# Kernel optimization log

Hardware: AMD Instinct MI355X
Metric: run time of the kernel (lower is better)

Reference implementation:

```python
import jax, jax.numpy as jnp
import numpy as np

D_MODEL = 512
D_STATE = 16
EXPAND = 2
DT_RANK = 8
D_INNER = EXPAND * D_MODEL  # 1024
LN_EPS = 1e-5


def setup_inputs() -> dict:
    key = jax.random.key(0)
    ks = jax.random.split(key, 10)
    B, H, W = 8, 48, 48
    inp = {
        "x": jax.random.normal(ks[0], (B, H, W, D_MODEL), jnp.float32),
        # Linear weights stored [in, out] (torch weight transposed)
        "W_in": jax.random.normal(ks[1], (D_MODEL, 2 * D_INNER), jnp.float32) * 0.02,
        # depthwise conv kernel, HWIO with feature_group_count = D_INNER
        "conv_k": jax.random.normal(ks[2], (3, 3, 1, D_INNER), jnp.float32) * 0.1,
        "W_xproj": jax.random.normal(ks[3], (D_INNER, DT_RANK + 2 * D_STATE), jnp.float32) * 0.02,
        "W_dt": jax.random.uniform(ks[4], (DT_RANK, D_INNER), jnp.float32, -0.1, 0.1),
        "b_dt": jnp.full((D_INNER,), 0.1, jnp.float32),
        "A_log": jax.random.normal(ks[5], (D_STATE,), jnp.float32) * 0.02,
        "Dskip": jnp.ones((D_INNER,), jnp.float32),
        "W_dtN": jax.random.normal(ks[6], (D_INNER, D_STATE), jnp.float32) * 0.02,
        "b_dtN": jnp.zeros((D_STATE,), jnp.float32),
        "ln_g": jnp.ones((D_INNER,), jnp.float32),
        "ln_b": jnp.zeros((D_INNER,), jnp.float32),
        "W_out": jax.random.normal(ks[7], (D_INNER, D_MODEL), jnp.float32) * 0.02,
        "b_out": jnp.zeros((D_MODEL,), jnp.float32),
    }
    return inp


def _ss2d(x, W_in, conv_k, W_xproj, W_dt, b_dt, A_log, Dskip, W_dtN, b_dtN,
          ln_g, ln_b, W_out, b_out):
    B, H, W_, _ = x.shape
    L = H * W_
    # in_proj and split into x / gate z
    xz = x @ W_in                                   # [B,H,W,2*D_INNER]
    xh, z = jnp.split(xz, 2, axis=-1)
    # depthwise 3x3 conv (NHWC)
    xc = jax.lax.conv_general_dilated(
        xh, conv_k, window_strides=(1, 1), padding='SAME',
        dimension_numbers=('NHWC', 'HWIO', 'NHWC'),
        feature_group_count=D_INNER)                 # [B,H,W,D_INNER]
    # x_proj -> (dt_rank, B, C)
    xp = xc @ W_xproj
    dt_r = xp[..., :DT_RANK]
    Bp = xp[..., DT_RANK:DT_RANK + D_STATE]
    Cp = xp[..., DT_RANK + D_STATE:]
    dt = dt_r @ W_dt + b_dt                          # [B,H,W,D_INNER]
    # flatten spatial dims into sequence
    x_seq = xc.reshape(B, L, D_INNER)
    dt_seq = jax.nn.softplus(dt.reshape(B, L, D_INNER))
    B_seq = Bp.reshape(B, L, D_STATE)
    C_seq = Cp.reshape(B, L, D_STATE)
    A = -jnp.exp(A_log)                              # [N]; A_log expanded over D is constant per-row
    dtN = dt_seq @ W_dtN + b_dtN                     # dt_to_N_proj(softplus(dt)) -> [B,L,N]

    def step(h, t):
        x_t, dt_t, dtN_t, B_t, C_t = t               # [B,D],[B,D],[B,N],[B,N],[B,N]
        dA = jnp.exp(dt_t[:, :, None] * A)           # [B,D,N]
        dB = dtN_t * B_t                             # [B,N]
        h = dA * h + dB[:, None, :] * x_t[:, :, None]  # [B,D,N]
        y = jnp.einsum('bdn,bn->bd', h, C_t) + Dskip * x_t
        return h, y

    h0 = jnp.zeros((B, D_INNER, D_STATE), x.dtype)
    xs = (x_seq.transpose(1, 0, 2), dt_seq.transpose(1, 0, 2),
          dtN.transpose(1, 0, 2), B_seq.transpose(1, 0, 2),
          C_seq.transpose(1, 0, 2))
    _, ys = jax.lax.scan(step, h0, xs)               # ys: [L,B,D]
    y = ys.transpose(1, 0, 2).reshape(B, H, W_, D_INNER)
    # LayerNorm over channel dim
    mu = y.mean(-1, keepdims=True)
    var = ((y - mu) ** 2).mean(-1, keepdims=True)
    y = (y - mu) / jnp.sqrt(var + LN_EPS) * ln_g + ln_b
    # gate and out projection (dropout = identity in eval)
    y = y * jax.nn.silu(z)
    return y @ W_out + b_out


def reference(x, W_in, conv_k, W_xproj, W_dt, b_dt, A_log, Dskip, W_dtN,
              b_dtN, ln_g, ln_b, W_out, b_out):
    return _ss2d(x, W_in, conv_k, W_xproj, W_dt, b_dt, A_log, Dskip, W_dtN,
                 b_dtN, ln_g, ln_b, W_out, b_out)
```

## Files before the change

### kernel.cpp

```cpp
#include <hip/hip_runtime.h>
#include <hip/hip_bf16.h>

#define NBATCH 8
#define HEIGHT 48
#define WIDTH  48
#define DMODEL 512
#define DSTATE 16
#define DTRANK 8
#define DINNER 1024
#define LSEQ   (HEIGHT*WIDTH)
#define NROWS  (NBATCH*LSEQ)
#define NXP    40
#define NCH    64
#define TCH    36

typedef unsigned short u16;
typedef unsigned int   u32;
typedef __attribute__((ext_vector_type(8))) short short8;
typedef __attribute__((ext_vector_type(4))) float f32x4;

__device__ __forceinline__ float bf2f(u16 u) {
    u32 x = ((u32)u) << 16;
    return __uint_as_float(x);
}
__device__ __forceinline__ u16 f2bf(float f) {
    u32 x = __float_as_uint(f);
    u32 r = (x + 0x7FFFu + ((x >> 16) & 1u)) >> 16;
    return (u16)r;
}

#if __has_builtin(__builtin_amdgcn_exp2f)
__device__ __forceinline__ float EXP2(float x) { return __builtin_amdgcn_exp2f(x); }
#else
__device__ __forceinline__ float EXP2(float x) { return __expf(x * 0.69314718f); }
#endif

#define GLD16(g, l) __builtin_amdgcn_global_load_lds( \
    (const __attribute__((address_space(1))) void*)(g), \
    (__attribute__((address_space(3))) void*)(l), 16, 0, 0)

__global__ __launch_bounds__(256) void k_prep(const float* __restrict__ x,
                                              const float* __restrict__ W_in,
                                              const float* __restrict__ W_out,
                                              const float* __restrict__ W_xproj,
                                              const float* __restrict__ W_dtN,
                                              u16* __restrict__ xbf,
                                              u16* __restrict__ WinT,
                                              u16* __restrict__ WoutT,
                                              u16* __restrict__ WxpB,
                                              u16* __restrict__ WdtNB) {
    if (blockIdx.x < 9216) {
        int i = blockIdx.x * 256 + threadIdx.x;
        float4 v = *reinterpret_cast<const float4*>(x + (size_t)i * 4);
        ushort4 o;
        o.x = f2bf(v.x); o.y = f2bf(v.y); o.z = f2bf(v.z); o.w = f2bf(v.w);
        *reinterpret_cast<ushort4*>(xbf + (size_t)i * 4) = o;
        return;
    }
    int idx = (blockIdx.x - 9216) * 256 + threadIdx.x;
    if (idx < 2048 * 512) {
        int n = idx >> 9, k = idx & 511;
        WinT[idx] = f2bf(W_in[(size_t)k * 2048 + n]);
    } else if (idx < 2048 * 512 + 512 * 1024) {
        int j = idx - 2048 * 512;
        int n = j >> 10, k = j & 1023;
        WoutT[j] = f2bf(W_out[(size_t)k * 512 + n]);
    } else if (idx < 2048 * 512 + 512 * 1024 + 48 * 1024) {
        int j = idx - (2048 * 512 + 512 * 1024);
        int n = j >> 10, k = j & 1023;
        WxpB[j] = (n < NXP) ? f2bf(W_xproj[(size_t)k * NXP + n]) : (u16)0;
    } else {
        int j = idx - (2048 * 512 + 512 * 1024 + 48 * 1024);
        int n = j >> 10, k = j & 1023;
        WdtNB[j] = f2bf(W_dtN[(size_t)k * DSTATE + n]);
    }
}

template<int K, int LDA, int LDB, int LDC, bool F32OUT>
__global__ __launch_bounds__(256) void k_gemm_mfma(const u16* __restrict__ A,
                                                   const u16* __restrict__ B,
                                                   const float* __restrict__ bias,
                                                   void* __restrict__ Cv) {
    __shared__ u16 As[128 * 32];
    __shared__ u16 Bs[128 * 32];
    const int tid = threadIdx.x;
    const int l   = tid & 63;
    const int w   = tid >> 6;
    const int wm  = w >> 1, wn = w & 1;
    const int id   = blockIdx.y * gridDim.x + blockIdx.x;
    const int nwg  = gridDim.x * gridDim.y;
    const int swz  = (id & 7) * (nwg >> 3) + (id >> 3);
    const int bx   = swz % gridDim.x;
    const int by   = swz / gridDim.x;
    const int m0  = by * 128, n0 = bx * 128;
    const int srow = w * 32 + (l >> 2);
    const int sc   = l & 3;
    const int kh = l >> 4;
    const int lr = l & 15;

    f32x4 acc[4][4];
#pragma unroll
    for (int i = 0; i < 4; ++i)
#pragma unroll
        for (int j = 0; j < 4; ++j)
            acc[i][j] = (f32x4){0.f, 0.f, 0.f, 0.f};

    for (int k0 = 0; k0 < K; k0 += 32) {
#pragma unroll
        for (int i = 0; i < 2; ++i) {
            int r  = srow + i * 16;
            int cg = sc ^ ((r >> 1) & 3);
            const u16* ga = A + (size_t)(m0 + r) * LDA + k0 + cg * 8;
            const u16* gb = B + (size_t)(n0 + r) * LDB + k0 + cg * 8;
            GLD16(ga, As + (w * 2 + i) * 512);
            GLD16(gb, Bs + (w * 2 + i) * 512);
        }
        __syncthreads();
        short8 af[4], bfr[4];
#pragma unroll
        for (int f = 0; f < 4; ++f) {
            int ar = wm * 64 + f * 16 + lr;
            af[f]  = *reinterpret_cast<const short8*>(As + ar * 32 + ((kh ^ ((ar >> 1) & 3)) * 8));
            int br = wn * 64 + f * 16 + lr;
            bfr[f] = *reinterpret_cast<const short8*>(Bs + br * 32 + ((kh ^ ((br >> 1) & 3)) * 8));
        }
#pragma unroll
        for (int fm = 0; fm < 4; ++fm)
#pragma unroll
            for (int fn = 0; fn < 4; ++fn)
                acc[fm][fn] = __builtin_amdgcn_mfma_f32_16x16x32_bf16(
                    af[fm], bfr[fn], acc[fm][fn], 0, 0, 0);
        __syncthreads();
    }

#pragma unroll
    for (int fm = 0; fm < 4; ++fm) {
#pragma unroll
        for (int r = 0; r < 4; ++r) {
            int row = m0 + wm * 64 + fm * 16 + (l >> 4) * 4 + r;
#pragma unroll
            for (int fn = 0; fn < 4; ++fn) {
                int col = n0 + wn * 64 + fn * 16 + lr;
                if (F32OUT) {
                    ((float*)Cv)[(size_t)row * LDC + col] = acc[fm][fn][r] + bias[col];
                } else {
                    ((u16*)Cv)[(size_t)row * LDC + col] = f2bf(acc[fm][fn][r]);
                }
            }
        }
    }
}

__global__ __launch_bounds__(256) void k_conv(const u16* __restrict__ xz,
                                              const float* __restrict__ ck,
                                              u16* __restrict__ xc) {
    const int blk = blockIdx.x;
    const int wg = blk % (WIDTH / 8);
    const int hb = blk / (WIDTH / 8);
    const int h = hb % HEIGHT;
    const int b = hb / HEIGHT;
    const int w0 = wg * 8;
    const int c0 = threadIdx.x * 4;

    float acc[8][4];
#pragma unroll
    for (int j = 0; j < 8; ++j)
#pragma unroll
        for (int q = 0; q < 4; ++q) acc[j][q] = 0.f;

#pragma unroll
    for (int kh = 0; kh < 3; ++kh) {
        int hh = h + kh - 1;
        if (hh < 0 || hh >= HEIGHT) continue;
        const u16* rp = xz + ((size_t)(b * HEIGHT + hh) * WIDTH) * 2048 + c0;
        float a[10][4];
#pragma unroll
        for (int i = 0; i < 10; ++i) {
            int ww = w0 - 1 + i;
            if (ww >= 0 && ww < WIDTH) {
                ushort4 v = *reinterpret_cast<const ushort4*>(rp + (size_t)ww * 2048);
                a[i][0] = bf2f(v.x); a[i][1] = bf2f(v.y);
                a[i][2] = bf2f(v.z); a[i][3] = bf2f(v.w);
            } else {
                a[i][0] = a[i][1] = a[i][2] = a[i][3] = 0.f;
            }
        }
#pragma unroll
        for (int kw = 0; kw < 3; ++kw) {
            float4 kv = *reinterpret_cast<const float4*>(ck + (kh * 3 + kw) * DINNER + c0);
#pragma unroll
            for (int j = 0; j < 8; ++j) {
                acc[j][0] = fmaf(a[j + kw][0], kv.x, acc[j][0]);
                acc[j][1] = fmaf(a[j + kw][1], kv.y, acc[j][1]);
                acc[j][2] = fmaf(a[j + kw][2], kv.z, acc[j][2]);
                acc[j][3] = fmaf(a[j + kw][3], kv.w, acc[j][3]);
            }
        }
    }
    const size_t orow = (size_t)((b * HEIGHT + h) * WIDTH + w0);
#pragma unroll
    for (int j = 0; j < 8; ++j) {
        ushort4 ov;
        ov.x = f2bf(acc[j][0]); ov.y = f2bf(acc[j][1]);
        ov.z = f2bf(acc[j][2]); ov.w = f2bf(acc[j][3]);
        *reinterpret_cast<ushort4*>(xc + (orow + j) * DINNER + c0) = ov;
    }
}

__global__ __launch_bounds__(256) void k_xproj(const u16* __restrict__ xc,
                                               const u16* __restrict__ WxpB,
                                               float* __restrict__ xp_out) {
    __shared__ u16 As[64 * 32];
    __shared__ u16 Bs[48 * 32];
    const int tid = threadIdx.x;
    const int l = tid & 63;
    const int w = tid >> 6;
    const int m0 = blockIdx.x * 64;
    const int kh = l >> 4, lr = l & 15;
    const int srow = w * 16 + (l >> 2);
    const int sc = l & 3;

    f32x4 acc[3];
    acc[0] = acc[1] = acc[2] = (f32x4){0.f, 0.f, 0.f, 0.f};

    for (int k0 = 0; k0 < 1024; k0 += 32) {
        {
            int cg = sc ^ ((srow >> 1) & 3);
            GLD16(xc + (size_t)(m0 + srow) * DINNER + k0 + cg * 8, As + w * 512);
            if (w < 3)
                GLD16(WxpB + (size_t)srow * 1024 + k0 + cg * 8, Bs + w * 512);
        }
        __syncthreads();
        int ar = w * 16 + lr;
        short8 af = *reinterpret_cast<const short8*>(As + ar * 32 + ((kh ^ ((ar >> 1) & 3)) * 8));
#pragma unroll
        for (int fn = 0; fn < 3; ++fn) {
            int br = fn * 16 + lr;
            short8 bf = *reinterpret_cast<const short8*>(Bs + br * 32 + ((kh ^ ((br >> 1) & 3)) * 8));
            acc[fn] = __builtin_amdgcn_mfma_f32_16x16x32_bf16(af, bf, acc[fn], 0, 0, 0);
        }
        __syncthreads();
    }
#pragma unroll
    for (int fn = 0; fn < 3; ++fn)
#pragma unroll
        for (int r = 0; r < 4; ++r) {
            int row = m0 + w * 16 + (l >> 4) * 4 + r;
            int col = fn * 16 + lr;
            if (col < NXP) xp_out[(size_t)row * NXP + col] = acc[fn][r];
        }
}

__global__ __launch_bounds__(256) void k_dt(const float* __restrict__ xp,
                                            const float* __restrict__ W_dt,
                                            const float* __restrict__ b_dt,
                                            u16* __restrict__ dt_out) {
    int gid = blockIdx.x * 256 + threadIdx.x;
    int row = gid >> 7;
    int dj  = (gid & 127) * 8;
    const float* xr = xp + (size_t)row * NXP;
    float4 xa = *reinterpret_cast<const float4*>(xr);
    float4 xb = *reinterpret_cast<const float4*>(xr + 4);
    float xv[8] = {xa.x, xa.y, xa.z, xa.w, xb.x, xb.y, xb.z, xb.w};
    float a[8];
    {
        float4 b0 = *reinterpret_cast<const float4*>(b_dt + dj);
        float4 b1 = *reinterpret_cast<const float4*>(b_dt + dj + 4);
        a[0]=b0.x; a[1]=b0.y; a[2]=b0.z; a[3]=b0.w;
        a[4]=b1.x; a[5]=b1.y; a[6]=b1.z; a[7]=b1.w;
    }
#pragma unroll
    for (int j = 0; j < 8; ++j) {
        float4 w0 = *reinterpret_cast<const float4*>(W_dt + j * DINNER + dj);
        float4 w1 = *reinterpret_cast<const float4*>(W_dt + j * DINNER + dj + 4);
        a[0] = fmaf(xv[j], w0.x, a[0]); a[1] = fmaf(xv[j], w0.y, a[1]);
        a[2] = fmaf(xv[j], w0.z, a[2]); a[3] = fmaf(xv[j], w0.w, a[3]);
        a[4] = fmaf(xv[j], w1.x, a[4]); a[5] = fmaf(xv[j], w1.y, a[5]);
        a[6] = fmaf(xv[j], w1.z, a[6]); a[7] = fmaf(xv[j], w1.w, a[7]);
    }
    short8 o;
#pragma unroll
    for (int j = 0; j < 8; ++j) {
        float dt = fmaxf(a[j], 0.f) + log1pf(__expf(-fabsf(a[j])));
        o[j] = (short)f2bf(dt);
    }
    *reinterpret_cast<short8*>(dt_out + (size_t)row * DINNER + dj) = o;
}

__global__ __launch_bounds__(256) void k_dtn(const u16* __restrict__ dtb,
                                             const u16* __restrict__ WdtNB,
                                             const float* __restrict__ b_dtN,
                                             const float* __restrict__ xp,
                                             float* __restrict__ dnBC) {
    __shared__ u16 As[64 * 32];
    __shared__ u16 Bs[16 * 32];
    const int tid = threadIdx.x;
    const int l = tid & 63;
    const int w = tid >> 6;
    const int m0 = blockIdx.x * 64;
    const int kh = l >> 4, lr = l & 15;
    const int srow = w * 16 + (l >> 2);
    const int sc = l & 3;

    f32x4 acc = (f32x4){0.f, 0.f, 0.f, 0.f};

    for (int k0 = 0; k0 < 1024; k0 += 32) {
        {
            int cg = sc ^ ((srow >> 1) & 3);
            GLD16(dtb + (size_t)(m0 + srow) * DINNER + k0 + cg * 8, As + w * 512);
            if (w == 0)
                GLD16(WdtNB + (size_t)srow * 1024 + k0 + cg * 8, Bs);
        }
        __syncthreads();
        int ar = w * 16 + lr;
        short8 af = *reinterpret_cast<const short8*>(As + ar * 32 + ((kh ^ ((ar >> 1) & 3)) * 8));
        short8 bf = *reinterpret_cast<const short8*>(Bs + lr * 32 + ((kh ^ ((lr >> 1) & 3)) * 8));
        acc = __builtin_amdgcn_mfma_f32_16x16x32_bf16(af, bf, acc, 0, 0, 0);
        __syncthreads();
    }
    float bn = b_dtN[lr];
#pragma unroll
    for (int r = 0; r < 4; ++r) {
        int row = m0 + w * 16 + (l >> 4) * 4 + r;
        float dn = acc[r] + bn;
        float Bv = xp[(size_t)row * NXP + DTRANK + lr];
        float Cv = xp[(size_t)row * NXP + DTRANK + DSTATE + lr];
        dnBC[(size_t)row * 32 + lr]      = dn * Bv;
        dnBC[(size_t)row * 32 + 16 + lr] = Cv;
    }
}

#define P1_N(IDX, COMP) \
    dA = EXP2(dt * An2[IDX]); h[IDX] = fmaf(dA, h[IDX], COMP * xt);

#define P1_BODY(T, DTC, XCC, DTN, XCN, PR) { \
    const float4* sv = pS + (size_t)(T) * 8; \
    float4 u0 = sv[0], u1 = sv[1], u2 = sv[2], u3 = sv[3]; \
    if (PR) { DTN = pdt[(size_t)((T) + 1) * DINNER]; \
              XCN = pxc[(size_t)((T) + 1) * DINNER]; } \
    float dt = bf2f(DTC), xt = bf2f(XCC); \
    sdt += dt; \
    float dA; \
    P1_N(0,  u0.x) P1_N(1,  u0.y) P1_N(2,  u0.z) P1_N(3,  u0.w) \
    P1_N(4,  u1.x) P1_N(5,  u1.y) P1_N(6,  u1.z) P1_N(7,  u1.w) \
    P1_N(8,  u2.x) P1_N(9,  u2.y) P1_N(10, u2.z) P1_N(11, u2.w) \
    P1_N(12, u3.x) P1_N(13, u3.y) P1_N(14, u3.z) P1_N(15, u3.w) }

__global__ __launch_bounds__(256) void k_scan_p1(const u16* __restrict__ xc,
                                                 const u16* __restrict__ dtb,
                                                 const float* __restrict__ dnBC,
                                                 const float* __restrict__ A_log,
                                                 float* __restrict__ sdt_out,
                                                 float* __restrict__ Qbuf) {
    const int tid = threadIdx.x;
    const int id  = blockIdx.x;
    const int swz = (id & 7) * ((NBATCH * NCH * 4) >> 3) + (id >> 3);
    const int quarter = swz & 3;
    const int bc = swz >> 2;
    const int c = bc & (NCH - 1);
    const int b = bc >> 6;
    const int d = quarter * 256 + tid;

    float An2[16];
#pragma unroll
    for (int n = 0; n < 16; ++n)
        An2[n] = -__expf(A_log[n]) * 1.44269504f;

    float h[16];
#pragma unroll
    for (int n = 0; n < 16; ++n) h[n] = 0.f;
    float sdt = 0.f;

    const size_t row0 = (size_t)b * LSEQ + (size_t)c * TCH;
    const u16* pdt = dtb + row0 * DINNER + d;
    const u16* pxc = xc  + row0 * DINNER + d;
    const float4* pS = reinterpret_cast<const float4*>(dnBC + row0 * 32);

    u16 dtA = pdt[0], xcA = pxc[0];
    u16 dtB, xcB;

    for (int t = 0; t < TCH - 2; t += 2) {
        P1_BODY(t,     dtA, xcA, dtB, xcB, true)
        P1_BODY(t + 1, dtB, xcB, dtA, xcA, true)
    }
    P1_BODY(TCH - 2, dtA, xcA, dtB, xcB, true)
    P1_BODY(TCH - 1, dtB, xcB, dtA, xcA, false)

    sdt_out[(size_t)bc * DINNER + d] = sdt;
    size_t base = ((size_t)bc << 14) + d;
#pragma unroll
    for (int n = 0; n < 16; ++n)
        Qbuf[base + (size_t)n * DINNER] = h[n];
}

__global__ __launch_bounds__(256) void k_scan_p2(const float* __restrict__ sdt,
                                                 const float* __restrict__ A_log,
                                                 float* __restrict__ Qbuf) {
    int tid = blockIdx.x * 256 + threadIdx.x;
    int b = tid >> 14, rem = tid & 16383;
    int n = rem >> 10, d = rem & 1023;
    float An2 = -__expf(A_log[n]) * 1.44269504f;
    float h = 0.f;
    for (int c = 0; c < NCH; ++c) {
        int bc = b * NCH + c;
        float P = EXP2(sdt[(size_t)bc * DINNER + d] * An2);
        size_t idx = ((size_t)bc << 14) + rem;
        float q = Qbuf[idx];
        Qbuf[idx] = h;
        h = fmaf(P, h, q);
    }
}

#define P3_N(IDX, UC, CC, YS) \
    dA = EXP2(dt * An2[IDX]); h[IDX] = fmaf(dA, h[IDX], UC * xt); \
    YS = fmaf(h[IDX], CC, YS);

#define P3_BODY(T, DTC, XCC, DTN, XCN, PR) { \
    const float4* sv = pS + (size_t)(T) * 8; \
    float4 u0 = sv[0], u1 = sv[1], u2 = sv[2], u3 = sv[3]; \
    float4 c4 = sv[4], c5 = sv[5], c6 = sv[6], c7 = sv[7]; \
    if (PR) { DTN = pdt[(size_t)((T) + 1) * DINNER]; \
              XCN = pxc[(size_t)((T) + 1) * DINNER]; } \
    float dt = bf2f(DTC), xt = bf2f(XCC); \
    float ys0 = Dsk * xt, ys1 = 0.f, ys2 = 0.f, ys3 = 0.f; \
    float dA; \
    P3_N(0,  u0.x, c4.x, ys0) P3_N(1,  u0.y, c4.y, ys1) \
    P3_N(2,  u0.z, c4.z, ys2) P3_N(3,  u0.w, c4.w, ys3) \
    P3_N(4,  u1.x, c5.x, ys0) P3_N(5,  u1.y, c5.y, ys1) \
    P3_N(6,  u1.z, c5.z, ys2) P3_N(7,  u1.w, c5.w, ys3) \
    P3_N(8,  u2.x, c6.x, ys0) P3_N(9,  u2.y, c6.y, ys1) \
    P3_N(10, u2.z, c6.z, ys2) P3_N(11, u2.w, c6.w, ys3) \
    P3_N(12, u3.x, c7.x, ys0) P3_N(13, u3.y, c7.y, ys1) \
    P3_N(14, u3.z, c7.z, ys2) P3_N(15, u3.w, c7.w, ys3) \
    ybuf[(row0 + (T)) * 2048 + d] = f2bf((ys0 + ys1) + (ys2 + ys3)); }

__global__ __launch_bounds__(256) void k_scan_p3(const u16* __restrict__ xc,
                                                 const u16* __restrict__ dtb,
                                                 const float* __restrict__ dnBC,
                                                 const float* __restrict__ A_log,
                                                 const float* __restrict__ Dskip,
                                                 const float* __restrict__ Qbuf,
                                                 u16* __restrict__ ybuf) {
    const int tid = threadIdx.x;
    const int id  = blockIdx.x;
    const int swz = (id & 7) * ((NBATCH * NCH * 4) >> 3) + (id >> 3);
    const int quarter = swz & 3;
    const int bc = swz >> 2;
    const int c = bc & (NCH - 1);
    const int b = bc >> 6;
    const int d = quarter * 256 + tid;

    float An2[16];
#pragma unroll
    for (int n = 0; n < 16; ++n)
        An2[n] = -__expf(A_log[n]) * 1.44269504f;

    float h[16];
    size_t base = ((size_t)bc << 14) + d;
#pragma unroll
    for (int n = 0; n < 16; ++n) h[n] = Qbuf[base + (size_t)n * DINNER];
    float Dsk = Dskip[d];

    const size_t row0 = (size_t)b * LSEQ + (size_t)c * TCH;
    const u16* pdt = dtb + row0 * DINNER + d;
    const u16* pxc = xc  + row0 * DINNER + d;
    const float4* pS = reinterpret_cast<const float4*>(dnBC + row0 * 32);

    u16 dtA = pdt[0], xcA = pxc[0];
    u16 dtB, xcB;

    for (int t = 0; t < TCH - 2; t += 2) {
        P3_BODY(t,     dtA, xcA, dtB, xcB, true)
        P3_BODY(t + 1, dtB, xcB, dtA, xcA, true)
    }
    P3_BODY(TCH - 2, dtA, xcA, dtB, xcB, true)
    P3_BODY(TCH - 1, dtB, xcB, dtA, xcA, false)
}

__global__ __launch_bounds__(256) void k_ln_gate(u16* __restrict__ xz,
                                                 const float* __restrict__ ln_g,
                                                 const float* __restrict__ ln_b) {
    __shared__ float red[8];
    int row = blockIdx.x, tid = threadIdx.x;
    u16* yrow = xz + (size_t)row * 2048;
    int c0 = tid * 4;
    ushort4 v = *reinterpret_cast<const ushort4*>(yrow + c0);
    float y0 = bf2f(v.x), y1 = bf2f(v.y), y2 = bf2f(v.z), y3 = bf2f(v.w);
    float s = y0 + y1 + y2 + y3;
    float q = y0 * y0 + y1 * y1 + y2 * y2 + y3 * y3;
#pragma unroll
    for (int m = 32; m; m >>= 1) {
        s += __shfl_xor(s, m, 64);
        q += __shfl_xor(q, m, 64);
    }
    int lane = tid & 63, wv = tid >> 6;
    if (lane == 0) { red[wv] = s; red[4 + wv] = q; }
    __syncthreads();
    s = red[0] + red[1] + red[2] + red[3];
    q = red[4] + red[5] + red[6] + red[7];
    float mu = s * (1.f / DINNER);
    float var = q * (1.f / DINNER) - mu * mu;
    float rstd = rsqrtf(var + 1e-5f);
    ushort4 zv = *reinterpret_cast<const ushort4*>(yrow + DINNER + c0);
    float4 lg = *reinterpret_cast<const float4*>(ln_g + c0);
    float4 lb = *reinterpret_cast<const float4*>(ln_b + c0);
    float z0 = bf2f(zv.x), z1 = bf2f(zv.y), z2 = bf2f(zv.z), z3 = bf2f(zv.w);
    float g0 = ((y0 - mu) * rstd * lg.x + lb.x) * (z0 / (1.f + __expf(-z0)));
    float g1 = ((y1 - mu) * rstd * lg.y + lb.y) * (z1 / (1.f + __expf(-z1)));
    float g2 = ((y2 - mu) * rstd * lg.z + lb.z) * (z2 / (1.f + __expf(-z2)));
    float g3 = ((y3 - mu) * rstd * lg.w + lb.w) * (z3 / (1.f + __expf(-z3)));
    ushort4 ov;
    ov.x = f2bf(g0); ov.y = f2bf(g1); ov.z = f2bf(g2); ov.w = f2bf(g3);
    *reinterpret_cast<ushort4*>(yrow + c0) = ov;
}

extern "C" void kernel_launch(void* const* d_in, const int* in_sizes, int n_in,
                              void* d_out, int out_size, void* d_ws, size_t ws_size,
                              hipStream_t stream) {
    const float* x       = (const float*)d_in[0];
    const float* W_in    = (const float*)d_in[1];
    const float* conv_k  = (const float*)d_in[2];
    const float* W_xproj = (const float*)d_in[3];
    const float* W_dt    = (const float*)d_in[4];
    const float* b_dt    = (const float*)d_in[5];
    const float* A_log   = (const float*)d_in[6];
    const float* Dskip   = (const float*)d_in[7];
    const float* W_dtN   = (const float*)d_in[8];
    const float* b_dtN   = (const float*)d_in[9];
    const float* ln_g    = (const float*)d_in[10];
    const float* ln_b    = (const float*)d_in[11];
    const float* W_out   = (const float*)d_in[12];
    const float* b_out   = (const float*)d_in[13];
    float* out = (float*)d_out;

    char* ws = (char*)d_ws;
    size_t off = 0;
    u16*   xz    = (u16*)(ws + off); off += (size_t)NROWS * 2048 * 2;
    u16*   xc    = (u16*)(ws + off); off += (size_t)NROWS * 1024 * 2;
    u16*   dtb   = (u16*)(ws + off); off += (size_t)NROWS * 1024 * 2;
    float* xpb   = (float*)(ws + off); off += (size_t)NROWS * NXP * 4;
    float* dnBC  = (float*)(ws + off); off += (size_t)NROWS * 32 * 4;
    char*  scr   = ws + off; off += (size_t)NBATCH * NCH * DINNER * DSTATE * 4;
    u16*   xbf   = (u16*)scr;
    float* Qbuf  = (float*)scr;
    float* sdtb  = xpb;
    u16*   WinT  = (u16*)(ws + off); off += (size_t)2048 * 512 * 2;
    u16*   WoutT = (u16*)(ws + off); off += (size_t)512 * 1024 * 2;
    u16*   WxpB  = (u16*)(ws + off); off += (size_t)48 * 1024 * 2;
    u16*   WdtNB = (u16*)(ws + off); off += (size_t)16 * 1024 * 2;

    k_prep<<<9216 + 6400, 256, 0, stream>>>(x, W_in, W_out, W_xproj, W_dtN,
                                            xbf, WinT, WoutT, WxpB, WdtNB);
    k_gemm_mfma<512, 512, 512, 2048, false>
        <<<dim3(2048 / 128, NROWS / 128), 256, 0, stream>>>(xbf, WinT, nullptr, xz);
    k_conv<<<NBATCH * HEIGHT * (WIDTH / 8), 256, 0, stream>>>(xz, conv_k, xc);
    k_xproj<<<NROWS / 64, 256, 0, stream>>>(xc, WxpB, xpb);
    k_dt<<<(NROWS * DINNER / 8) / 256, 256, 0, stream>>>(xpb, W_dt, b_dt, dtb);
    k_dtn<<<NROWS / 64, 256, 0, stream>>>(dtb, WdtNB, b_dtN, xpb, dnBC);
    k_scan_p1<<<NBATCH * NCH * 4, 256, 0, stream>>>(xc, dtb, dnBC, A_log,
                                                    sdtb, Qbuf);
    k_scan_p2<<<(NBATCH * DINNER * DSTATE) / 256, 256, 0, stream>>>(sdtb, A_log, Qbuf);
    k_scan_p3<<<NBATCH * NCH * 4, 256, 0, stream>>>(xc, dtb, dnBC, A_log,
                                                    Dskip, Qbuf, xz);
    k_ln_gate<<<NROWS, 256, 0, stream>>>(xz, ln_g, ln_b);
    k_gemm_mfma<1024, 2048, 1024, 512, true>
        <<<dim3(DMODEL / 128, NROWS / 128), 256, 0, stream>>>(xz, WoutT, b_out, out);
}
```

Baseline: 328.5 us.

## Compute two conv rows per block, store scan carries in bf16, wave-per-row layernorm

The depthwise conv now produces two output rows per block, so the overlapping input rows are loaded once and reused, cutting input reads from 3 to 4 rows per 2 outputs. The chunked-scan carry buffer (Qbuf) is stored in bf16 instead of fp32, halving traffic between the three scan phases at the cost of precision in the inter-chunk states. The layernorm+gate kernel maps one wavefront to each row with 16-element vector loads, removing the shared-memory reduction and block barrier. The scratch region is resized to match.

```diff
diff --git a/kernel.cpp b/kernel.cpp
--- a/kernel.cpp
+++ b/kernel.cpp
@@ -156,54 +156,63 @@
                                               u16* __restrict__ xc) {
     const int blk = blockIdx.x;
     const int wg = blk % (WIDTH / 8);
-    const int hb = blk / (WIDTH / 8);
-    const int h = hb % HEIGHT;
-    const int b = hb / HEIGHT;
+    const int rest = blk / (WIDTH / 8);
+    const int hp = rest % (HEIGHT / 2);
+    const int b = rest / (HEIGHT / 2);
+    const int h0 = hp * 2;
     const int w0 = wg * 8;
     const int c0 = threadIdx.x * 4;
 
-    float acc[8][4];
-#pragma unroll
-    for (int j = 0; j < 8; ++j)
+    float acc[16][4];
+#pragma unroll
+    for (int j = 0; j < 16; ++j)
 #pragma unroll
         for (int q = 0; q < 4; ++q) acc[j][q] = 0.f;
 
 #pragma unroll
-    for (int kh = 0; kh < 3; ++kh) {
-        int hh = h + kh - 1;
+    for (int i = 0; i < 4; ++i) {
+        int hh = h0 - 1 + i;
         if (hh < 0 || hh >= HEIGHT) continue;
         const u16* rp = xz + ((size_t)(b * HEIGHT + hh) * WIDTH) * 2048 + c0;
         float a[10][4];
 #pragma unroll
-        for (int i = 0; i < 10; ++i) {
-            int ww = w0 - 1 + i;
+        for (int p = 0; p < 10; ++p) {
+            int ww = w0 - 1 + p;
             if (ww >= 0 && ww < WIDTH) {
                 ushort4 v = *reinterpret_cast<const ushort4*>(rp + (size_t)ww * 2048);
-                a[i][0] = bf2f(v.x); a[i][1] = bf2f(v.y);
-                a[i][2] = bf2f(v.z); a[i][3] = bf2f(v.w);
+                a[p][0] = bf2f(v.x); a[p][1] = bf2f(v.y);
+                a[p][2] = bf2f(v.z); a[p][3] = bf2f(v.w);
             } else {
-                a[i][0] = a[i][1] = a[i][2] = a[i][3] = 0.f;
+                a[p][0] = a[p][1] = a[p][2] = a[p][3] = 0.f;
             }
         }
 #pragma unroll
-        for (int kw = 0; kw < 3; ++kw) {
-            float4 kv = *reinterpret_cast<const float4*>(ck + (kh * 3 + kw) * DINNER + c0);
-#pragma unroll
-            for (int j = 0; j < 8; ++j) {
-                acc[j][0] = fmaf(a[j + kw][0], kv.x, acc[j][0]);
-                acc[j][1] = fmaf(a[j + kw][1], kv.y, acc[j][1]);
-                acc[j][2] = fmaf(a[j + kw][2], kv.z, acc[j][2]);
-                acc[j][3] = fmaf(a[j + kw][3], kv.w, acc[j][3]);
+        for (int oh = 0; oh < 2; ++oh) {
+            int kh = i - oh;
+            if (kh < 0 || kh > 2) continue;
+#pragma unroll
+            for (int kw = 0; kw < 3; ++kw) {
+                float4 kv = *reinterpret_cast<const float4*>(ck + (kh * 3 + kw) * DINNER + c0);
+#pragma unroll
+                for (int j = 0; j < 8; ++j) {
+                    acc[oh * 8 + j][0] = fmaf(a[j + kw][0], kv.x, acc[oh * 8 + j][0]);
+                    acc[oh * 8 + j][1] = fmaf(a[j + kw][1], kv.y, acc[oh * 8 + j][1]);
+                    acc[oh * 8 + j][2] = fmaf(a[j + kw][2], kv.z, acc[oh * 8 + j][2]);
+                    acc[oh * 8 + j][3] = fmaf(a[j + kw][3], kv.w, acc[oh * 8 + j][3]);
+                }
             }
         }
     }
-    const size_t orow = (size_t)((b * HEIGHT + h) * WIDTH + w0);
-#pragma unroll
-    for (int j = 0; j < 8; ++j) {
-        ushort4 ov;
-        ov.x = f2bf(acc[j][0]); ov.y = f2bf(acc[j][1]);
-        ov.z = f2bf(acc[j][2]); ov.w = f2bf(acc[j][3]);
-        *reinterpret_cast<ushort4*>(xc + (orow + j) * DINNER + c0) = ov;
+#pragma unroll
+    for (int oh = 0; oh < 2; ++oh) {
+        const size_t orow = (size_t)((b * HEIGHT + h0 + oh) * WIDTH + w0);
+#pragma unroll
+        for (int j = 0; j < 8; ++j) {
+            ushort4 ov;
+            ov.x = f2bf(acc[oh * 8 + j][0]); ov.y = f2bf(acc[oh * 8 + j][1]);
+            ov.z = f2bf(acc[oh * 8 + j][2]); ov.w = f2bf(acc[oh * 8 + j][3]);
+            *reinterpret_cast<ushort4*>(xc + (orow + j) * DINNER + c0) = ov;
+        }
     }
 }
 
@@ -351,7 +360,7 @@
                                                  const float* __restrict__ dnBC,
                                                  const float* __restrict__ A_log,
                                                  float* __restrict__ sdt_out,
-                                                 float* __restrict__ Qbuf) {
+                                                 u16* __restrict__ Qbuf) {
     const int tid = threadIdx.x;
     const int id  = blockIdx.x;
     const int swz = (id & 7) * ((NBATCH * NCH * 4) >> 3) + (id >> 3);
@@ -390,12 +399,12 @@
     size_t base = ((size_t)bc << 14) + d;
 #pragma unroll
     for (int n = 0; n < 16; ++n)
-        Qbuf[base + (size_t)n * DINNER] = h[n];
+        Qbuf[base + (size_t)n * DINNER] = f2bf(h[n]);
 }
 
 __global__ __launch_bounds__(256) void k_scan_p2(const float* __restrict__ sdt,
                                                  const float* __restrict__ A_log,
-                                                 float* __restrict__ Qbuf) {
+                                                 u16* __restrict__ Qbuf) {
     int tid = blockIdx.x * 256 + threadIdx.x;
     int b = tid >> 14, rem = tid & 16383;
     int n = rem >> 10, d = rem & 1023;
@@ -405,8 +414,8 @@
         int bc = b * NCH + c;
         float P = EXP2(sdt[(size_t)bc * DINNER + d] * An2);
         size_t idx = ((size_t)bc << 14) + rem;
-        float q = Qbuf[idx];
-        Qbuf[idx] = h;
+        float q = bf2f(Qbuf[idx]);
+        Qbuf[idx] = f2bf(h);
         h = fmaf(P, h, q);
     }
 }
@@ -439,7 +448,7 @@
                                                  const float* __restrict__ dnBC,
                                                  const float* __restrict__ A_log,
                                                  const float* __restrict__ Dskip,
-                                                 const float* __restrict__ Qbuf,
+                                                 const u16* __restrict__ Qbuf,
                                                  u16* __restrict__ ybuf) {
     const int tid = threadIdx.x;
     const int id  = blockIdx.x;
@@ -458,7 +467,7 @@
     float h[16];
     size_t base = ((size_t)bc << 14) + d;
 #pragma unroll
-    for (int n = 0; n < 16; ++n) h[n] = Qbuf[base + (size_t)n * DINNER];
+    for (int n = 0; n < 16; ++n) h[n] = bf2f(Qbuf[base + (size_t)n * DINNER]);
     float Dsk = Dskip[d];
 
     const size_t row0 = (size_t)b * LSEQ + (size_t)c * TCH;
@@ -480,38 +489,55 @@
 __global__ __launch_bounds__(256) void k_ln_gate(u16* __restrict__ xz,
                                                  const float* __restrict__ ln_g,
                                                  const float* __restrict__ ln_b) {
-    __shared__ float red[8];
-    int row = blockIdx.x, tid = threadIdx.x;
+    const int wv = threadIdx.x >> 6, l = threadIdx.x & 63;
+    const int row = blockIdx.x * 4 + wv;
     u16* yrow = xz + (size_t)row * 2048;
-    int c0 = tid * 4;
-    ushort4 v = *reinterpret_cast<const ushort4*>(yrow + c0);
-    float y0 = bf2f(v.x), y1 = bf2f(v.y), y2 = bf2f(v.z), y3 = bf2f(v.w);
-    float s = y0 + y1 + y2 + y3;
-    float q = y0 * y0 + y1 * y1 + y2 * y2 + y3 * y3;
+    const int c0 = l * 16;
+
+    short8 v0 = *reinterpret_cast<const short8*>(yrow + c0);
+    short8 v1 = *reinterpret_cast<const short8*>(yrow + c0 + 8);
+    float y[16];
+#pragma unroll
+    for (int j = 0; j < 8; ++j) {
+        y[j]     = bf2f((u16)v0[j]);
+        y[8 + j] = bf2f((u16)v1[j]);
+    }
+    float s = 0.f, q = 0.f;
+#pragma unroll
+    for (int j = 0; j < 16; ++j) { s += y[j]; q = fmaf(y[j], y[j], q); }
 #pragma unroll
     for (int m = 32; m; m >>= 1) {
         s += __shfl_xor(s, m, 64);
         q += __shfl_xor(q, m, 64);
     }
-    int lane = tid & 63, wv = tid >> 6;
-    if (lane == 0) { red[wv] = s; red[4 + wv] = q; }
-    __syncthreads();
-    s = red[0] + red[1] + red[2] + red[3];
-    q = red[4] + red[5] + red[6] + red[7];
     float mu = s * (1.f / DINNER);
     float var = q * (1.f / DINNER) - mu * mu;
     float rstd = rsqrtf(var + 1e-5f);
-    ushort4 zv = *reinterpret_cast<const ushort4*>(yrow + DINNER + c0);
-    float4 lg = *reinterpret_cast<const float4*>(ln_g + c0);
-    float4 lb = *reinterpret_cast<const float4*>(ln_b + c0);
-    float z0 = bf2f(zv.x), z1 = bf2f(zv.y), z2 = bf2f(zv.z), z3 = bf2f(zv.w);
-    float g0 = ((y0 - mu) * rstd * lg.x + lb.x) * (z0 / (1.f + __expf(-z0)));
-    float g1 = ((y1 - mu) * rstd * lg.y + lb.y) * (z1 / (1.f + __expf(-z1)));
-    float g2 = ((y2 - mu) * rstd * lg.z + lb.z) * (z2 / (1.f + __expf(-z2)));
-    float g3 = ((y3 - mu) * rstd * lg.w + lb.w) * (z3 / (1.f + __expf(-z3)));
-    ushort4 ov;
-    ov.x = f2bf(g0); ov.y = f2bf(g1); ov.z = f2bf(g2); ov.w = f2bf(g3);
-    *reinterpret_cast<ushort4*>(yrow + c0) = ov;
+
+    short8 z0 = *reinterpret_cast<const short8*>(yrow + DINNER + c0);
+    short8 z1 = *reinterpret_cast<const short8*>(yrow + DINNER + c0 + 8);
+    float4 lg0 = *reinterpret_cast<const float4*>(ln_g + c0);
+    float4 lg1 = *reinterpret_cast<const float4*>(ln_g + c0 + 4);
+    float4 lg2 = *reinterpret_cast<const float4*>(ln_g + c0 + 8);
+    float4 lg3 = *reinterpret_cast<const float4*>(ln_g + c0 + 12);
+    float4 lb0 = *reinterpret_cast<const float4*>(ln_b + c0);
+    float4 lb1 = *reinterpret_cast<const float4*>(ln_b + c0 + 4);
+    float4 lb2 = *reinterpret_cast<const float4*>(ln_b + c0 + 8);
+    float4 lb3 = *reinterpret_cast<const float4*>(ln_b + c0 + 12);
+    float lg[16] = {lg0.x,lg0.y,lg0.z,lg0.w, lg1.x,lg1.y,lg1.z,lg1.w,
+                    lg2.x,lg2.y,lg2.z,lg2.w, lg3.x,lg3.y,lg3.z,lg3.w};
+    float lb[16] = {lb0.x,lb0.y,lb0.z,lb0.w, lb1.x,lb1.y,lb1.z,lb1.w,
+                    lb2.x,lb2.y,lb2.z,lb2.w, lb3.x,lb3.y,lb3.z,lb3.w};
+
+    short8 o0, o1;
+#pragma unroll
+    for (int j = 0; j < 16; ++j) {
+        float zv = bf2f((u16)((j < 8) ? z0[j] : z1[j - 8]));
+        float g = ((y[j] - mu) * rstd * lg[j] + lb[j]) * (zv / (1.f + __expf(-zv)));
+        if (j < 8) o0[j] = (short)f2bf(g); else o1[j - 8] = (short)f2bf(g);
+    }
+    *reinterpret_cast<short8*>(yrow + c0)     = o0;
+    *reinterpret_cast<short8*>(yrow + c0 + 8) = o1;
 }
 
 extern "C" void kernel_launch(void* const* d_in, const int* in_sizes, int n_in,
@@ -540,9 +566,9 @@
     u16*   dtb   = (u16*)(ws + off); off += (size_t)NROWS * 1024 * 2;
     float* xpb   = (float*)(ws + off); off += (size_t)NROWS * NXP * 4;
     float* dnBC  = (float*)(ws + off); off += (size_t)NROWS * 32 * 4;
-    char*  scr   = ws + off; off += (size_t)NBATCH * NCH * DINNER * DSTATE * 4;
+    char*  scr   = ws + off; off += (size_t)NROWS * DMODEL * 2;
     u16*   xbf   = (u16*)scr;
-    float* Qbuf  = (float*)scr;
+    u16*   Qbuf  = (u16*)scr;
     float* sdtb  = xpb;
     u16*   WinT  = (u16*)(ws + off); off += (size_t)2048 * 512 * 2;
     u16*   WoutT = (u16*)(ws + off); off += (size_t)512 * 1024 * 2;
@@ -553,7 +579,7 @@
                                             xbf, WinT, WoutT, WxpB, WdtNB);
     k_gemm_mfma<512, 512, 512, 2048, false>
         <<<dim3(2048 / 128, NROWS / 128), 256, 0, stream>>>(xbf, WinT, nullptr, xz);
-    k_conv<<<NBATCH * HEIGHT * (WIDTH / 8), 256, 0, stream>>>(xz, conv_k, xc);
+    k_conv<<<NBATCH * (HEIGHT / 2) * (WIDTH / 8), 256, 0, stream>>>(xz, conv_k, xc);
     k_xproj<<<NROWS / 64, 256, 0, stream>>>(xc, WxpB, xpb);
     k_dt<<<(NROWS * DINNER / 8) / 256, 256, 0, stream>>>(xpb, W_dt, b_dt, dtb);
     k_dtn<<<NROWS / 64, 256, 0, stream>>>(dtb, WdtNB, b_dtN, xpb, dnBC);
@@ -562,7 +588,7 @@
     k_scan_p2<<<(NBATCH * DINNER * DSTATE) / 256, 256, 0, stream>>>(sdtb, A_log, Qbuf);
     k_scan_p3<<<NBATCH * NCH * 4, 256, 0, stream>>>(xc, dtb, dnBC, A_log,
                                                     Dskip, Qbuf, xz);
-    k_ln_gate<<<NROWS, 256, 0, stream>>>(xz, ln_g, ln_b);
+    k_ln_gate<<<NROWS / 4, 256, 0, stream>>>(xz, ln_g, ln_b);
     k_gemm_mfma<1024, 2048, 1024, 512, true>
         <<<dim3(DMODEL / 128, NROWS / 128), 256, 0, stream>>>(xz, WoutT, b_out, out);
 }
```

After: 325.6 us, median of 2. No clear change (-0.9%).
